# Optimization experiments

Hardware: AMD Instinct MI355X
Metric: run time of the kernel (lower is better)

Reference implementation:

```python
import jax, jax.numpy as jnp
import numpy as np

TOP_K = 8
NUM_EXPERTS = 256
HIDDEN = 7168
NUM_TOKENS = 16384
NORM_TOPK_PROB = True


def setup_inputs() -> dict:
    key = jax.random.key(0)
    k1, k2 = jax.random.split(key)
    hidden_states = jax.random.normal(k1, (NUM_TOKENS, HIDDEN), dtype=jnp.float32)
    weight = jax.random.normal(k2, (NUM_EXPERTS, HIDDEN), dtype=jnp.float32) * 0.02
    return {"hidden_states": hidden_states, "weight": weight}


def reference(hidden_states, weight):
    # Router logits: [T, E] = [T, H] @ [E, H]^T
    logits = jnp.einsum("th,eh->te", hidden_states, weight)
    # Fused softmax + top-k (npu_moe_gating_top_k_softmax semantics):
    # softmax over experts, then take top-k probabilities and their indices.
    probs = jax.nn.softmax(logits, axis=-1)
    topk_weight, topk_idx = jax.lax.top_k(probs, TOP_K)  # [T, k]
    # row_idx: expert-major (column-major) flattened row indices, as the NPU op returns.
    T = logits.shape[0]
    row_idx = jnp.arange(T * TOP_K, dtype=jnp.int32).reshape(TOP_K, T).T  # [T, k]
    if TOP_K > 1 and NORM_TOPK_PROB:
        denominator = jnp.sum(topk_weight, axis=-1, keepdims=True) + 1e-20
        topk_weight = topk_weight / denominator
    topk_idx = topk_idx.astype(jnp.int32)
    return (topk_idx, topk_weight, row_idx)
```

## Files before the change

kernel.cpp:

```cpp
#include <hip/hip_runtime.h>
#include <hip/hip_bf16.h>

#define NTOK 16384
#define HID 7168
#define NEXP 256
#define TOPK 8

#define BT 32
#define NIT 112

typedef __bf16 bf16x8 __attribute__((ext_vector_type(8)));
typedef float  f32x16 __attribute__((ext_vector_type(16)));

__device__ __align__(16) unsigned short g_wb[NEXP * HID];

__device__ __forceinline__ unsigned int f2bfb(float x) {
    unsigned int u = __float_as_uint(x);
    return (u + 0x7fffu + ((u >> 16) & 1u)) >> 16;
}
__device__ __forceinline__ uint4 pk4(float4 p, float4 q) {
    uint4 u;
    u.x = f2bfb(p.x) | (f2bfb(p.y) << 16);
    u.y = f2bfb(p.z) | (f2bfb(p.w) << 16);
    u.z = f2bfb(q.x) | (f2bfb(q.y) << 16);
    u.w = f2bfb(q.z) | (f2bfb(q.w) << 16);
    return u;
}
__device__ __forceinline__ bf16x8 asbf8(uint4 u) {
    union { uint4 a; bf16x8 b; } c; c.a = u; return c.b;
}

__global__ void wconv_frag(const float* __restrict__ wt) {
    const int tid = blockIdx.x * 256 + threadIdx.x;
    const int l  = tid & 63;
    const int ks = (tid >> 6) & 7;
    const int g  = (tid >> 9) & 7;
    const int p  = tid >> 12;
    const int e  = g * 32 + (l & 31);
    const int kb = p * 128 + ks * 16 + ((l >> 5) << 3);
    const float4* s = (const float4*)(wt + (size_t)e * HID + kb);
    ((uint4*)g_wb)[tid] = pk4(s[0], s[1]);
}

__global__ void moe_rows(float* __restrict__ ob) {
    const int q = blockIdx.x * 256 + threadIdx.x;
    ob[262144 + q] = (float)((q & 7) * NTOK + (q >> 3));
}

__device__ __forceinline__ void softbar() {
    asm volatile("s_waitcnt lgkmcnt(0)" ::: "memory");
    __builtin_amdgcn_s_barrier();
    __builtin_amdgcn_sched_barrier(0);
}

__global__ __launch_bounds__(512, 4) void moe_gate_v22(
    const float* __restrict__ hs,
    float* __restrict__ ob)
{
    __shared__ __align__(16) char smem[33792];

    const int tid   = threadIdx.x;
    const int lane  = tid & 63;
    const int w     = tid >> 6;
    const int khalf = lane >> 5;
    const int t0    = blockIdx.x * BT;

    const int ar = tid >> 4;
    const int ac = tid & 15;
    const float* aload = hs + (size_t)(t0 + ar) * HID + ac * 4;
    const int awb = (ac >> 1) * 512 + ar * 16 + (ac & 1) * 8;

    const int arb = (lane & 31) * 16;

    const char* const bbase = (const char*)g_wb + w * 8192 + lane * 16;

    f32x16 acc = {};
    uint4 bA0, bA1, bA2, bA3;
    uint4 bB0, bB1, bB2, bB3;

    char* p0 = smem;
    char* p1 = smem + 4096;
    char* p2 = smem + 8192;

#define LOADB(SET, S)                                                         \
    do {                                                                      \
        const char* bp = bbase + (size_t)((S) >> 1) * 65536 + ((S) & 1) * 4096; \
        b##SET##0 = *(const uint4*)(bp);                                      \
        b##SET##1 = *(const uint4*)(bp + 1024);                               \
        b##SET##2 = *(const uint4*)(bp + 2048);                               \
        b##SET##3 = *(const uint4*)(bp + 3072);                               \
    } while (0)

#define WRITEA(V, BUF)                                                        \
    do {                                                                      \
        uint2 u;                                                              \
        u.x = f2bfb((V).x) | (f2bfb((V).y) << 16);                            \
        u.y = f2bfb((V).z) | (f2bfb((V).w) << 16);                            \
        *(uint2*)((BUF) + awb) = u;                                           \
    } while (0)

#define COMPUTE(BUF, SET)                                                     \
    do {                                                                      \
        bf16x8 a;                                                             \
        a = *(const bf16x8*)((BUF) + (0 * 2 + khalf) * 512 + arb);            \
        acc = __builtin_amdgcn_mfma_f32_32x32x16_bf16(a, asbf8(b##SET##0), acc, 0, 0, 0); \
        a = *(const bf16x8*)((BUF) + (1 * 2 + khalf) * 512 + arb);            \
        acc = __builtin_amdgcn_mfma_f32_32x32x16_bf16(a, asbf8(b##SET##1), acc, 0, 0, 0); \
        a = *(const bf16x8*)((BUF) + (2 * 2 + khalf) * 512 + arb);            \
        acc = __builtin_amdgcn_mfma_f32_32x32x16_bf16(a, asbf8(b##SET##2), acc, 0, 0, 0); \
        a = *(const bf16x8*)((BUF) + (3 * 2 + khalf) * 512 + arb);            \
        acc = __builtin_amdgcn_mfma_f32_32x32x16_bf16(a, asbf8(b##SET##3), acc, 0, 0, 0); \
    } while (0)

    {
        float4 v0 = *(const float4*)(aload);
        float4 v1 = *(const float4*)(aload + 64);
        WRITEA(v0, p0);
        WRITEA(v1, p1);
    }
    LOADB(A, 0);
    softbar();

    for (int s = 0; s < NIT; s += 2) {
        float4 vA;
        const bool ldA = (s + 2 < NIT);
        if (ldA) vA = *(const float4*)(aload + (size_t)(s + 2) * 64);
        LOADB(B, s + 1);
        COMPUTE(p0, A);
        softbar();
        if (ldA) WRITEA(vA, p2);

        float4 vB;
        const bool ldB = (s + 3 < NIT);
        if (ldB) vB = *(const float4*)(aload + (size_t)(s + 3) * 64);
        if (s + 2 < NIT) LOADB(A, s + 2);
        COMPUTE(p1, B);
        softbar();
        if (ldB) WRITEA(vB, p0);

        char* t = p2; p2 = p1; p1 = p0; p0 = t;
    }

    __syncthreads();

    float* ll = (float*)smem;
    {
        const int ec = w * 32 + (lane & 31);
        #pragma unroll
        for (int r = 0; r < 16; ++r) {
            const int tok = (r & 3) + 8 * (r >> 2) + 4 * khalf;
            ll[tok * 257 + ec] = acc[r];
        }
    }
    __syncthreads();

    if (tid < BT) {
        const float* lr = ll + tid * 257;
        float bv[TOPK]; int bi8[TOPK];
        #pragma unroll
        for (int k = 0; k < TOPK; ++k) { bv[k] = -1e30f; bi8[k] = 0; }
        for (int e = 0; e < NEXP; ++e) {
            const float v = lr[e];
            if (v > bv[TOPK - 1]) {
                int k = TOPK - 1;
                while (k > 0 && v > bv[k - 1]) {
                    bv[k] = bv[k - 1]; bi8[k] = bi8[k - 1]; --k;
                }
                bv[k] = v; bi8[k] = e;
            }
        }
        float ev[TOPK], ssum = 0.f;
        #pragma unroll
        for (int r = 0; r < TOPK; ++r) { ev[r] = expf(bv[r] - bv[0]); ssum += ev[r]; }
        const float inv = 1.0f / ssum;

        const int tg = t0 + tid;
        #pragma unroll
        for (int r = 0; r < TOPK; ++r) {
            ob[(size_t)tg * TOPK + r]          = (float)bi8[r];
            ob[131072 + (size_t)tg * TOPK + r] = ev[r] * inv;
        }
    }
#undef LOADB
#undef WRITEA
#undef COMPUTE
}

extern "C" void kernel_launch(void* const* d_in, const int* in_sizes, int n_in,
                              void* d_out, int out_size, void* d_ws, size_t ws_size,
                              hipStream_t stream) {
    const float* hs = (const float*)d_in[0];
    const float* wt = (const float*)d_in[1];
    float* ob = (float*)d_out;

    wconv_frag<<<dim3(NEXP * HID / 8 / 256), dim3(256), 0, stream>>>(wt);
    moe_gate_v22<<<dim3(NTOK / BT), dim3(512), 0, stream>>>(hs, ob);
    moe_rows<<<dim3(512), dim3(256), 0, stream>>>(ob);
}
```

Baseline: 245.0 us.

## Split-K router GEMM with LDS-resident weight slices and separate reduce/top-k kernel

Restructures the GEMM as a split-K over 28 slices of 256 hidden elements. Each block loads its whole bf16 weight slice into LDS once via global_load_lds and then streams 1024 tokens through it, writing bf16 partial logits to the workspace. A new reduce kernel sums the partials across slices and does the top-k softmax. This removes the repeated per-block weight reads from global memory, but adds a large partial-sum round trip through memory (28 × T × E bf16) and bf16 rounding of the partials. Occupancy also drops to one block per CU because of the 144KB LDS footprint.

Measured after the change: 340.0 us. 1.39x slower.

```diff
diff --git a/kernel.cpp b/kernel.cpp
--- a/kernel.cpp
+++ b/kernel.cpp
@@ -5,14 +5,16 @@
 #define HID 7168
 #define NEXP 256
 #define TOPK 8
-
-#define BT 32
-#define NIT 112
+#define KSL 256
+#define NKZ 28
+#define NIT 32
 
 typedef __bf16 bf16x8 __attribute__((ext_vector_type(8)));
 typedef float  f32x16 __attribute__((ext_vector_type(16)));
-
-__device__ __align__(16) unsigned short g_wb[NEXP * HID];
+typedef __attribute__((address_space(1))) const unsigned char ga_t;
+typedef __attribute__((address_space(3))) unsigned char la_t;
+
+__device__ __align__(16) unsigned short g_wb2[NEXP * HID];
 
 __device__ __forceinline__ unsigned int f2bfb(float x) {
     unsigned int u = __float_as_uint(x);
@@ -26,20 +28,26 @@
     u.w = f2bfb(q.z) | (f2bfb(q.w) << 16);
     return u;
 }
-__device__ __forceinline__ bf16x8 asbf8(uint4 u) {
-    union { uint4 a; bf16x8 b; } c; c.a = u; return c.b;
-}
-
-__global__ void wconv_frag(const float* __restrict__ wt) {
-    const int tid = blockIdx.x * 256 + threadIdx.x;
-    const int l  = tid & 63;
-    const int ks = (tid >> 6) & 7;
-    const int g  = (tid >> 9) & 7;
-    const int p  = tid >> 12;
-    const int e  = g * 32 + (l & 31);
-    const int kb = p * 128 + ks * 16 + ((l >> 5) << 3);
-    const float4* s = (const float4*)(wt + (size_t)e * HID + kb);
-    ((uint4*)g_wb)[tid] = pk4(s[0], s[1]);
+__device__ __forceinline__ void gll16(const void* g, void* l) {
+    __builtin_amdgcn_global_load_lds((ga_t*)g, (la_t*)l, 16, 0, 0);
+}
+
+__global__ void wconv2(const float* __restrict__ wt) {
+    const int id = blockIdx.x * 256 + threadIdx.x;
+    const int ku = id & 31;
+    const int e  = (id >> 5) & 255;
+    const int kz = id >> 13;
+    const float* s = wt + (size_t)e * HID + kz * KSL + ku * 8;
+    const float4 f0 = *(const float4*)(s);
+    const float4 f1 = *(const float4*)(s + 4);
+    uint2 o;
+    o.x = f2bfb(f0.x) | (f2bfb(f0.y) << 16);
+    o.y = f2bfb(f0.z) | (f2bfb(f0.w) << 16);
+    uint2 o2;
+    o2.x = f2bfb(f1.x) | (f2bfb(f1.y) << 16);
+    o2.y = f2bfb(f1.z) | (f2bfb(f1.w) << 16);
+    uint4 u = make_uint4(o.x, o.y, o2.x, o2.y);
+    ((uint4*)g_wb2)[(size_t)kz * 8192 + (size_t)ku * 256 + e] = u;
 }
 
 __global__ void moe_rows(float* __restrict__ ob) {
@@ -53,108 +61,141 @@
     __builtin_amdgcn_sched_barrier(0);
 }
 
-__global__ __launch_bounds__(512, 4) void moe_gate_v22(
+__global__ __launch_bounds__(512, 1) void moe_gate_v23(
     const float* __restrict__ hs,
+    unsigned short* __restrict__ pw)
+{
+    __shared__ __align__(16) char smem[147456];
+
+    const int tid   = threadIdx.x;
+    const int lane  = tid & 63;
+    const int l31   = lane & 31;
+    const int khalf = lane >> 5;
+    const int w     = tid >> 6;
+    const int t0    = blockIdx.x * 1024;
+    const int kz    = blockIdx.y;
+
+    {
+        const char* bsrc = (const char*)g_wb2 + (size_t)kz * 131072;
+        #pragma unroll
+        for (int j = 0; j < 16; ++j)
+            gll16(bsrc + (size_t)(tid + j * 512) * 16, smem + (tid + j * 512) * 16);
+    }
+    __syncthreads();
+
+    const int r  = tid >> 4;
+    const int kc = tid & 15;
+    const float* aptr = hs + (size_t)(t0 + r) * HID + kz * KSL + kc * 16;
+    const int awb0 = 131072 + (2 * kc) * 512 + r * 16;
+    const int awb1 = awb0 + 512;
+
+    const int abase = 131072 + l31 * 16;
+    const int bbase = (w * 32 + l31) * 16;
+
+    float4 fa0, fa1, fa2, fa3;
+    float4 fb0, fb1, fb2, fb3;
+
+#define LOADA(S, IT)                                                          \
+    do {                                                                      \
+        const float* p = aptr + (size_t)(IT) * 32 * HID;                      \
+        f##S##0 = *(const float4*)(p);                                        \
+        f##S##1 = *(const float4*)(p + 4);                                    \
+        f##S##2 = *(const float4*)(p + 8);                                    \
+        f##S##3 = *(const float4*)(p + 12);                                   \
+    } while (0)
+
+#define WRITEA(S)                                                             \
+    do {                                                                      \
+        *(uint4*)(smem + awb0) = pk4(f##S##0, f##S##1);                       \
+        *(uint4*)(smem + awb1) = pk4(f##S##2, f##S##3);                       \
+    } while (0)
+
+#define TILE(ACC)                                                             \
+    do {                                                                      \
+        _Pragma("unroll")                                                     \
+        for (int s = 0; s < 16; ++s) {                                        \
+            const int ku = 2 * s + khalf;                                     \
+            bf16x8 a = *(const bf16x8*)(smem + abase + ku * 512);             \
+            bf16x8 b = *(const bf16x8*)(smem + bbase + ku * 4096);            \
+            ACC = __builtin_amdgcn_mfma_f32_32x32x16_bf16(a, b, ACC, 0, 0, 0);\
+        }                                                                     \
+    } while (0)
+
+#define STOREP(ACC, IT)                                                       \
+    do {                                                                      \
+        _Pragma("unroll")                                                     \
+        for (int q = 0; q < 16; ++q) {                                        \
+            const float o = __shfl_xor(ACC[q], 1);                            \
+            if (!(lane & 1)) {                                                \
+                const unsigned int v = f2bfb(ACC[q]) | (f2bfb(o) << 16);      \
+                const int tokl = (q & 3) + 8 * (q >> 2) + 4 * khalf;          \
+                ((unsigned int*)pw)[(size_t)kz * 2097152                      \
+                    + (size_t)(t0 + (IT) * 32 + tokl) * 128                   \
+                    + ((w * 32 + l31) >> 1)] = v;                             \
+            }                                                                 \
+        }                                                                     \
+    } while (0)
+
+    LOADA(a, 0);
+    WRITEA(a);
+    softbar();
+
+    for (int it = 0; it < NIT; it += 2) {
+        LOADA(b, it + 1);
+        {
+            f32x16 acc = {};
+            TILE(acc);
+            STOREP(acc, it);
+        }
+        softbar();
+        WRITEA(b);
+        softbar();
+
+        if (it + 2 < NIT) LOADA(a, it + 2);
+        {
+            f32x16 acc = {};
+            TILE(acc);
+            STOREP(acc, it + 1);
+        }
+        softbar();
+        if (it + 2 < NIT) {
+            WRITEA(a);
+            softbar();
+        }
+    }
+#undef LOADA
+#undef WRITEA
+#undef TILE
+#undef STOREP
+}
+
+__global__ __launch_bounds__(256) void moe_reduce2(
+    const unsigned short* __restrict__ pw,
     float* __restrict__ ob)
 {
-    __shared__ __align__(16) char smem[33792];
-
-    const int tid   = threadIdx.x;
-    const int lane  = tid & 63;
-    const int w     = tid >> 6;
-    const int khalf = lane >> 5;
-    const int t0    = blockIdx.x * BT;
-
-    const int ar = tid >> 4;
-    const int ac = tid & 15;
-    const float* aload = hs + (size_t)(t0 + ar) * HID + ac * 4;
-    const int awb = (ac >> 1) * 512 + ar * 16 + (ac & 1) * 8;
-
-    const int arb = (lane & 31) * 16;
-
-    const char* const bbase = (const char*)g_wb + w * 8192 + lane * 16;
-
-    f32x16 acc = {};
-    uint4 bA0, bA1, bA2, bA3;
-    uint4 bB0, bB1, bB2, bB3;
-
-    char* p0 = smem;
-    char* p1 = smem + 4096;
-    char* p2 = smem + 8192;
-
-#define LOADB(SET, S)                                                         \
-    do {                                                                      \
-        const char* bp = bbase + (size_t)((S) >> 1) * 65536 + ((S) & 1) * 4096; \
-        b##SET##0 = *(const uint4*)(bp);                                      \
-        b##SET##1 = *(const uint4*)(bp + 1024);                               \
-        b##SET##2 = *(const uint4*)(bp + 2048);                               \
-        b##SET##3 = *(const uint4*)(bp + 3072);                               \
-    } while (0)
-
-#define WRITEA(V, BUF)                                                        \
-    do {                                                                      \
-        uint2 u;                                                              \
-        u.x = f2bfb((V).x) | (f2bfb((V).y) << 16);                            \
-        u.y = f2bfb((V).z) | (f2bfb((V).w) << 16);                            \
-        *(uint2*)((BUF) + awb) = u;                                           \
-    } while (0)
-
-#define COMPUTE(BUF, SET)                                                     \
-    do {                                                                      \
-        bf16x8 a;                                                             \
-        a = *(const bf16x8*)((BUF) + (0 * 2 + khalf) * 512 + arb);            \
-        acc = __builtin_amdgcn_mfma_f32_32x32x16_bf16(a, asbf8(b##SET##0), acc, 0, 0, 0); \
-        a = *(const bf16x8*)((BUF) + (1 * 2 + khalf) * 512 + arb);            \
-        acc = __builtin_amdgcn_mfma_f32_32x32x16_bf16(a, asbf8(b##SET##1), acc, 0, 0, 0); \
-        a = *(const bf16x8*)((BUF) + (2 * 2 + khalf) * 512 + arb);            \
-        acc = __builtin_amdgcn_mfma_f32_32x32x16_bf16(a, asbf8(b##SET##2), acc, 0, 0, 0); \
-        a = *(const bf16x8*)((BUF) + (3 * 2 + khalf) * 512 + arb);            \
-        acc = __builtin_amdgcn_mfma_f32_32x32x16_bf16(a, asbf8(b##SET##3), acc, 0, 0, 0); \
-    } while (0)
-
-    {
-        float4 v0 = *(const float4*)(aload);
-        float4 v1 = *(const float4*)(aload + 64);
-        WRITEA(v0, p0);
-        WRITEA(v1, p1);
-    }
-    LOADB(A, 0);
-    softbar();
-
-    for (int s = 0; s < NIT; s += 2) {
-        float4 vA;
-        const bool ldA = (s + 2 < NIT);
-        if (ldA) vA = *(const float4*)(aload + (size_t)(s + 2) * 64);
-        LOADB(B, s + 1);
-        COMPUTE(p0, A);
-        softbar();
-        if (ldA) WRITEA(vA, p2);
-
-        float4 vB;
-        const bool ldB = (s + 3 < NIT);
-        if (ldB) vB = *(const float4*)(aload + (size_t)(s + 3) * 64);
-        if (s + 2 < NIT) LOADB(A, s + 2);
-        COMPUTE(p1, B);
-        softbar();
-        if (ldB) WRITEA(vB, p0);
-
-        char* t = p2; p2 = p1; p1 = p0; p0 = t;
-    }
-
+    __shared__ float ll[64 * 257];
+    const int tid = threadIdx.x;
+    const size_t ro = (size_t)blockIdx.x * 16384;
+
+    #pragma unroll
+    for (int j = 0; j < 16; ++j) {
+        const int f = j * 1024 + tid * 4;
+        float4 v = make_float4(0.f, 0.f, 0.f, 0.f);
+        #pragma unroll
+        for (int kzi = 0; kzi < NKZ; ++kzi) {
+            const uint2 u = *(const uint2*)(pw + (size_t)kzi * 4194304 + ro + f);
+            v.x += __uint_as_float((u.x & 0xffffu) << 16);
+            v.y += __uint_as_float(u.x & 0xffff0000u);
+            v.z += __uint_as_float((u.y & 0xffffu) << 16);
+            v.w += __uint_as_float(u.y & 0xffff0000u);
+        }
+        const int t = f >> 8;
+        const int e = f & 255;
+        *(float4*)&ll[t * 257 + e] = v;
+    }
     __syncthreads();
 
-    float* ll = (float*)smem;
-    {
-        const int ec = w * 32 + (lane & 31);
-        #pragma unroll
-        for (int r = 0; r < 16; ++r) {
-            const int tok = (r & 3) + 8 * (r >> 2) + 4 * khalf;
-            ll[tok * 257 + ec] = acc[r];
-        }
-    }
-    __syncthreads();
-
-    if (tid < BT) {
+    if (tid < 64) {
         const float* lr = ll + tid * 257;
         float bv[TOPK]; int bi8[TOPK];
         #pragma unroll
@@ -171,19 +212,16 @@
         }
         float ev[TOPK], ssum = 0.f;
         #pragma unroll
-        for (int r = 0; r < TOPK; ++r) { ev[r] = expf(bv[r] - bv[0]); ssum += ev[r]; }
+        for (int q = 0; q < TOPK; ++q) { ev[q] = expf(bv[q] - bv[0]); ssum += ev[q]; }
         const float inv = 1.0f / ssum;
 
-        const int tg = t0 + tid;
-        #pragma unroll
-        for (int r = 0; r < TOPK; ++r) {
-            ob[(size_t)tg * TOPK + r]          = (float)bi8[r];
-            ob[131072 + (size_t)tg * TOPK + r] = ev[r] * inv;
-        }
-    }
-#undef LOADB
-#undef WRITEA
-#undef COMPUTE
+        const int tg = blockIdx.x * 64 + tid;
+        #pragma unroll
+        for (int q = 0; q < TOPK; ++q) {
+            ob[(size_t)tg * TOPK + q]          = (float)bi8[q];
+            ob[131072 + (size_t)tg * TOPK + q] = ev[q] * inv;
+        }
+    }
 }
 
 extern "C" void kernel_launch(void* const* d_in, const int* in_sizes, int n_in,
@@ -192,8 +230,10 @@
     const float* hs = (const float*)d_in[0];
     const float* wt = (const float*)d_in[1];
     float* ob = (float*)d_out;
-
-    wconv_frag<<<dim3(NEXP * HID / 8 / 256), dim3(256), 0, stream>>>(wt);
-    moe_gate_v22<<<dim3(NTOK / BT), dim3(512), 0, stream>>>(hs, ob);
+    unsigned short* pw = (unsigned short*)d_ws;
+
+    wconv2<<<dim3(NEXP * HID / 8 / 256), dim3(256), 0, stream>>>(wt);
+    moe_gate_v23<<<dim3(16, NKZ), dim3(512), 0, stream>>>(hs, pw);
+    moe_reduce2<<<dim3(256), dim3(256), 0, stream>>>(pw, ob);
     moe_rows<<<dim3(512), dim3(256), 0, stream>>>(ob);
 }
```
